# Kernel optimization log

Measured on AMD Instinct MI355X. Metric: run time of the kernel, lower is better.

The kernel has to match this reference:

```python
import jax, jax.numpy as jnp
import numpy as np

NODE_DIM = 512
HIDDEN = 4096
N_NODES = 4096  # must equal HIDDEN for pool Linear to typecheck (as in source)
N_EDGES = 131072


def setup_inputs() -> dict:
    key = jax.random.key(0)
    ks = jax.random.split(key, 12)
    s1 = 0.02
    x = jax.random.normal(ks[0], (N_NODES, NODE_DIM), dtype=jnp.float32)
    edge_index = jax.random.randint(ks[1], (2, N_EDGES), 0, N_NODES, dtype=jnp.int64)
    # encoder: Linear(node_dim, hidden) -> ReLU -> Linear(hidden, hidden)
    W1 = jax.random.normal(ks[2], (NODE_DIM, HIDDEN), dtype=jnp.float32) * s1
    b1 = jnp.zeros((HIDDEN,), dtype=jnp.float32)
    W2 = jax.random.normal(ks[3], (HIDDEN, HIDDEN), dtype=jnp.float32) * s1
    b2 = jnp.zeros((HIDDEN,), dtype=jnp.float32)
    # pool: Linear(hidden, hidden) -> ReLU -> Linear(hidden, 1)
    W3 = jax.random.normal(ks[4], (HIDDEN, HIDDEN), dtype=jnp.float32) * s1
    b3 = jnp.zeros((HIDDEN,), dtype=jnp.float32)
    W4 = jax.random.normal(ks[5], (HIDDEN, 1), dtype=jnp.float32) * s1
    b4 = jnp.zeros((1,), dtype=jnp.float32)
    return {"x": x, "edge_index": edge_index, "W1": W1, "b1": b1,
            "W2": W2, "b2": b2, "W3": W3, "b3": b3, "W4": W4, "b4": b4}


def reference(x, edge_index, W1, b1, W2, b2, W3, b3, W4, b4):
    # encoder MLP: [N, node_dim] -> [N, hidden]
    h = jax.nn.relu(x @ W1 + b1) @ W2 + b2
    # kernel_vector = (h @ h.T).sum(1) == h @ h.sum(0)  (avoids O(N^2) Gram)
    s = h.sum(axis=0)                 # [hidden]
    kernel_vector = h @ s             # [N]
    kv = kernel_vector[None, :]       # [1, N] with N == hidden
    pooled = jax.nn.relu(kv @ W3 + b3) @ W4 + b4   # [1, 1]
    return pooled
```

## Files before the change

kernel.cpp:

```cpp
#include <hip/hip_runtime.h>

#define NODES 4096
#define NDIM  512
#define HID   4096

typedef __attribute__((ext_vector_type(8))) short bf16x8;
typedef __attribute__((ext_vector_type(4))) float f32x4;

__device__ __forceinline__ float b2f(short v) {
  union { unsigned int u; float f; } c;
  c.u = ((unsigned int)(unsigned short)v) << 16;
  return c.f;
}
__device__ __forceinline__ short f2b(float f) {
  union { float f; unsigned int u; } c; c.f = f;
  unsigned int r = c.u + 0x7fffu + ((c.u >> 16) & 1u);
  return (short)(r >> 16);
}

__global__ __launch_bounds__(256) void k_prep(const float* __restrict__ x,
                                              const float* __restrict__ W1,
                                              const float* __restrict__ b2,
                                              const float* __restrict__ b3,
                                              short* __restrict__ xb,
                                              short* __restrict__ w1t,
                                              float* __restrict__ aacc,
                                              float* __restrict__ svec,
                                              float* __restrict__ uacc) {
  __shared__ float tile[32][33];
  int b = blockIdx.x;
  if (b < 2048) {
    int i = (b * 256 + threadIdx.x) * 4;
    float4 v = *(const float4*)(x + i);
    short4 o;
    o.x = f2b(v.x); o.y = f2b(v.y); o.z = f2b(v.z); o.w = f2b(v.w);
    *(short4*)(xb + i) = o;
  } else if (b < 4096) {
    int t = b - 2048;
    int n0 = (t & 127) * 32;
    int k0 = (t >> 7) * 32;
    int tx = threadIdx.x & 31, ty = threadIdx.x >> 5;
    #pragma unroll
    for (int j = 0; j < 4; ++j) {
      int kk = ty + j * 8;
      tile[kk][tx] = W1[(size_t)(k0 + kk) * HID + n0 + tx];
    }
    __syncthreads();
    #pragma unroll
    for (int j = 0; j < 4; ++j) {
      int nn = ty + j * 8;
      w1t[(size_t)(n0 + nn) * NDIM + k0 + tx] = f2b(tile[tx][nn]);
    }
  } else {
    int j = (b - 4096) * 256 + threadIdx.x;
    aacc[j] = 0.0f;
    svec[j] = (float)NODES * b2[j];
    uacc[j] = b3[j];
  }
}

__global__ __launch_bounds__(512, 2) void k_gemm1(const short* __restrict__ xb,
                                                  const short* __restrict__ w1t,
                                                  const float* __restrict__ b1,
                                                  short* __restrict__ Aout,
                                                  float* __restrict__ colsum) {
  extern __shared__ char smem[];
  __shared__ float csum[256];

  const int tid  = threadIdx.x;
  const int lane = tid & 63;
  const int wid  = tid >> 6;
  const int wr   = wid >> 2;
  const int wc   = wid & 3;

  int bswz = (blockIdx.x & 7) * 32 + (blockIdx.x >> 3);
  const int brow = (bswz >> 4) * 256, bcol = (bswz & 15) * 256;

  f32x4 acc[8][4];
  #pragma unroll
  for (int i = 0; i < 8; ++i)
    #pragma unroll
    for (int j = 0; j < 4; ++j)
      acc[i][j] = (f32x4){0.f, 0.f, 0.f, 0.f};

  if (tid < 256) csum[tid] = 0.f;

  const int fr = lane & 15;
  const int fko = ((lane >> 4) ^ ((lane >> 1) & 3)) * 8;

  const int off0 = tid * 16;
  const int row0 = off0 >> 6;
  const int gs   = (off0 >> 4) & 3;
  const int ce0  = (gs ^ ((row0 >> 1) & 3)) * 8;
  const short* gA0 = xb  + (size_t)(brow + row0) * NDIM + ce0;
  const short* gA1 = xb  + (size_t)(brow + row0 + 128) * NDIM + ce0;
  const short* gB0 = w1t + (size_t)(bcol + row0) * NDIM + ce0;
  const short* gB1 = w1t + (size_t)(bcol + row0 + 128) * NDIM + ce0;

#define GLOAD(src, dst) __builtin_amdgcn_global_load_lds( \
    (const __attribute__((address_space(1))) void*)(src), \
    (__attribute__((address_space(3))) void*)(dst), 16, 0, 0)

#define STAGE_HALF(buf, tile_, kh) do { \
    char* bA_ = smem + (buf) * 32768 + (kh) * 16384; \
    char* bB_ = smem + 65536 + (buf) * 32768 + (kh) * 16384; \
    int ks_ = (tile_) * 64 + (kh) * 32; \
    GLOAD(gA0 + ks_, bA_ + off0); \
    GLOAD(gA1 + ks_, bA_ + off0 + 8192); \
    GLOAD(gB0 + ks_, bB_ + off0); \
    GLOAD(gB1 + ks_, bB_ + off0 + 8192); \
  } while (0)

#define DS_BFR(buf, kh) do { \
    const short* Bb_ = (const short*)(smem + 65536 + (buf) * 32768 + (kh) * 16384); \
    _Pragma("unroll") \
    for (int ni = 0; ni < 4; ++ni) \
      bfr[ni] = *(const bf16x8*)(Bb_ + (wc * 64 + ni * 16 + fr) * 32 + fko); \
  } while (0)

#define DS_AF(buf, kh, mh) do { \
    const short* Ab_ = (const short*)(smem + (buf) * 32768 + (kh) * 16384); \
    _Pragma("unroll") \
    for (int mi = 0; mi < 4; ++mi) \
      af[mi] = *(const bf16x8*)(Ab_ + (wr * 128 + ((mh) * 4 + mi) * 16 + fr) * 32 + fko); \
  } while (0)

#define MFMA16(mh) do { \
    __builtin_amdgcn_s_setprio(1); \
    _Pragma("unroll") \
    for (int mi = 0; mi < 4; ++mi) \
      _Pragma("unroll") \
      for (int ni = 0; ni < 4; ++ni) \
        acc[(mh) * 4 + mi][ni] = __builtin_amdgcn_mfma_f32_16x16x32_bf16( \
            bfr[ni], af[mi], acc[(mh) * 4 + mi][ni], 0, 0, 0); \
    __builtin_amdgcn_s_setprio(0); \
  } while (0)

#define BAR() __builtin_amdgcn_s_barrier()
#define LGKM0() asm volatile("s_waitcnt lgkmcnt(0)" ::: "memory")
#define WCNT(s) asm volatile("s_waitcnt " s ::: "memory")

#define ITER(kk, DO_S0, DO_S2, V1, V3) do { \
    int b_ = (kk) & 1; \
    bf16x8 af[4], bfr[4]; \
     \
    if (DO_S0) STAGE_HALF(((kk) + 1) & 1, (kk) + 1, 1); \
    DS_BFR(b_, 0); DS_AF(b_, 0, 0); \
    BAR(); LGKM0(); \
    MFMA16(0); \
    BAR(); \
     \
    DS_AF(b_, 0, 1); \
    BAR(); LGKM0(); \
    MFMA16(1); \
    WCNT(V1); BAR(); \
     \
    if (DO_S2) STAGE_HALF(b_, (kk) + 2, 0); \
    DS_BFR(b_, 1); DS_AF(b_, 1, 0); \
    BAR(); LGKM0(); \
    MFMA16(0); \
    BAR(); \
     \
    DS_AF(b_, 1, 1); \
    BAR(); LGKM0(); \
    MFMA16(1); \
    WCNT(V3); BAR(); \
  } while (0)

  STAGE_HALF(0, 0, 0);
  STAGE_HALF(0, 0, 1);
  STAGE_HALF(1, 1, 0);
  WCNT("vmcnt(8)");
  BAR();

  #pragma unroll 1
  for (int kt = 0; kt < 6; ++kt)
    ITER(kt, true, true, "vmcnt(8)", "vmcnt(8)");
  ITER(6, true, false, "vmcnt(8)", "vmcnt(4)");
  ITER(7, false, false, "vmcnt(0)", "vmcnt(0)");

  const int cr = lane & 15;
  const int cg = (lane >> 4) * 4;
  float4 bias4[4];
  #pragma unroll
  for (int ni = 0; ni < 4; ++ni)
    bias4[ni] = *(const float4*)(b1 + bcol + wc * 64 + ni * 16 + cg);

  float cl[4][4];
  #pragma unroll
  for (int ni = 0; ni < 4; ++ni)
    #pragma unroll
    for (int r = 0; r < 4; ++r)
      cl[ni][r] = 0.f;

  short* pk = (short*)smem;
  #pragma unroll 1
  for (int half = 0; half < 2; ++half) {
    __syncthreads();
    if (wr == half) {
      #pragma unroll
      for (int mi = 0; mi < 8; ++mi) {
        int lrow = mi * 16 + cr;
        #pragma unroll
        for (int ni = 0; ni < 4; ++ni) {
          float v0 = fmaxf(acc[mi][ni][0] + bias4[ni].x, 0.f);
          float v1 = fmaxf(acc[mi][ni][1] + bias4[ni].y, 0.f);
          float v2 = fmaxf(acc[mi][ni][2] + bias4[ni].z, 0.f);
          float v3 = fmaxf(acc[mi][ni][3] + bias4[ni].w, 0.f);
          cl[ni][0] += v0; cl[ni][1] += v1; cl[ni][2] += v2; cl[ni][3] += v3;
          short4 o;
          o.x = f2b(v0); o.y = f2b(v1); o.z = f2b(v2); o.w = f2b(v3);
          *(short4*)(pk + lrow * 264 + wc * 64 + ni * 16 + cg) = o;
        }
      }
    }
    __syncthreads();
    #pragma unroll
    for (int i = 0; i < 8; ++i) {
      int c = tid + i * 512;
      int row = c >> 5, ch = c & 31;
      bf16x8 vv = *(const bf16x8*)(pk + row * 264 + ch * 8);
      *(bf16x8*)(Aout + (size_t)(brow + half * 128 + row) * HID + bcol + ch * 8) = vv;
    }
  }

  #pragma unroll
  for (int ni = 0; ni < 4; ++ni)
    #pragma unroll
    for (int r = 0; r < 4; ++r) {
      #pragma unroll
      for (int m = 1; m < 16; m <<= 1)
        cl[ni][r] += __shfl_xor(cl[ni][r], m);
    }
  if (cr == 0) {
    #pragma unroll
    for (int ni = 0; ni < 4; ++ni)
      #pragma unroll
      for (int r = 0; r < 4; ++r)
        atomicAdd(&csum[wc * 64 + ni * 16 + cg + r], cl[ni][r]);
  }
  __syncthreads();
  if (tid < 256) atomicAdd(&colsum[bcol + tid], csum[tid]);
}

__global__ __launch_bounds__(256) void k_gemv_at(const float* __restrict__ W,
                                                 const float* __restrict__ vin,
                                                 float* __restrict__ vout) {
  const int col = blockIdx.x * 1024 + threadIdx.x * 4;
  const int r0  = blockIdx.y * 64;
  float4 accv = {0.f, 0.f, 0.f, 0.f};
  const float* base = W + (size_t)r0 * HID + col;
  #pragma unroll 16
  for (int i = 0; i < 64; ++i) {
    float vi = vin[r0 + i];
    float4 wv = *(const float4*)(base + (size_t)i * HID);
    accv.x += vi * wv.x; accv.y += vi * wv.y;
    accv.z += vi * wv.z; accv.w += vi * wv.w;
  }
  atomicAdd(&vout[col + 0], accv.x);
  atomicAdd(&vout[col + 1], accv.y);
  atomicAdd(&vout[col + 2], accv.z);
  atomicAdd(&vout[col + 3], accv.w);
}

__global__ __launch_bounds__(256) void k_gemv_row(const float* __restrict__ W,
                                                  const float* __restrict__ vin,
                                                  const float* __restrict__ b2,
                                                  float* __restrict__ vout,
                                                  float* __restrict__ beta) {
  __shared__ float red[4];
  if (blockIdx.x == HID / 4) {
    float p = 0.f;
    for (int j = threadIdx.x; j < HID; j += 256) p += b2[j] * vin[j];
    #pragma unroll
    for (int o = 32; o > 0; o >>= 1) p += __shfl_down(p, o);
    int lane = threadIdx.x & 63, w = threadIdx.x >> 6;
    if (lane == 0) red[w] = p;
    __syncthreads();
    if (threadIdx.x == 0) beta[0] = red[0] + red[1] + red[2] + red[3];
    return;
  }
  int w = threadIdx.x >> 6, lane = threadIdx.x & 63;
  int row = blockIdx.x * 4 + w;
  const float* base = W + (size_t)row * HID;
  float p = 0.f;
  #pragma unroll 8
  for (int j = lane * 4; j < HID; j += 256) {
    float4 wv = *(const float4*)(base + j);
    float4 sv = *(const float4*)(vin + j);
    p += wv.x * sv.x + wv.y * sv.y + wv.z * sv.z + wv.w * sv.w;
  }
  #pragma unroll
  for (int o = 32; o > 0; o >>= 1) p += __shfl_down(p, o);
  if (lane == 0) vout[row] = p;
}

__global__ __launch_bounds__(256) void k_kv(const short* __restrict__ A,
                                            const float* __restrict__ t,
                                            const float* __restrict__ beta,
                                            float* __restrict__ kv) {
  int w = threadIdx.x >> 6, lane = threadIdx.x & 63;
  int row = blockIdx.x * 4 + w;
  const short* base = A + (size_t)row * HID;
  float p = 0.f;
  #pragma unroll
  for (int j = lane * 8; j < HID; j += 512) {
    bf16x8 av = *(const bf16x8*)(base + j);
    float4 t0 = *(const float4*)(t + j);
    float4 t1 = *(const float4*)(t + j + 4);
    p += b2f(av[0]) * t0.x + b2f(av[1]) * t0.y + b2f(av[2]) * t0.z + b2f(av[3]) * t0.w
       + b2f(av[4]) * t1.x + b2f(av[5]) * t1.y + b2f(av[6]) * t1.z + b2f(av[7]) * t1.w;
  }
  #pragma unroll
  for (int o = 32; o > 0; o >>= 1) p += __shfl_down(p, o);
  if (lane == 0) kv[row] = p + beta[0];
}

__global__ __launch_bounds__(256) void k_final(const float* __restrict__ uacc,
                                               const float* __restrict__ W4,
                                               const float* __restrict__ b4,
                                               float* __restrict__ out) {
  __shared__ float red[4];
  float p = 0.f;
  for (int j = threadIdx.x; j < HID; j += 256) {
    float uv = uacc[j];
    uv = uv > 0.f ? uv : 0.f;
    p += uv * W4[j];
  }
  #pragma unroll
  for (int o = 32; o > 0; o >>= 1) p += __shfl_down(p, o);
  int lane = threadIdx.x & 63, w = threadIdx.x >> 6;
  if (lane == 0) red[w] = p;
  __syncthreads();
  if (threadIdx.x == 0) out[0] = red[0] + red[1] + red[2] + red[3] + b4[0];
}

extern "C" void kernel_launch(void* const* d_in, const int* in_sizes, int n_in,
                              void* d_out, int out_size, void* d_ws, size_t ws_size,
                              hipStream_t stream) {
  const float* x  = (const float*)d_in[0];
  const float* W1 = (const float*)d_in[2];
  const float* b1 = (const float*)d_in[3];
  const float* W2 = (const float*)d_in[4];
  const float* b2 = (const float*)d_in[5];
  const float* W3 = (const float*)d_in[6];
  const float* b3 = (const float*)d_in[7];
  const float* W4 = (const float*)d_in[8];
  const float* b4 = (const float*)d_in[9];
  float* out = (float*)d_out;

  char* ws = (char*)d_ws;
  short* Abf  = (short*)(ws);
  short* xb   = (short*)(ws + 33554432);
  short* w1t  = (short*)(ws + 37748736);
  float* aacc = (float*)(ws + 41943040);
  float* svec = (float*)(ws + 41959424);
  float* tvec = (float*)(ws + 41975808);
  float* kvv  = (float*)(ws + 41992192);
  float* uacc = (float*)(ws + 42008576);
  float* beta = (float*)(ws + 42024960);

  k_prep    <<<dim3(4112),     dim3(256), 0, stream>>>(x, W1, b2, b3, xb, w1t, aacc, svec, uacc);
  k_gemm1   <<<dim3(256),      dim3(512), 131072, stream>>>(xb, w1t, b1, Abf, aacc);
  k_gemv_at <<<dim3(4, 64),    dim3(256), 0, stream>>>(W2, aacc, svec);
  k_gemv_row<<<dim3(1025),     dim3(256), 0, stream>>>(W2, svec, b2, tvec, beta);
  k_kv      <<<dim3(1024),     dim3(256), 0, stream>>>(Abf, tvec, beta, kvv);
  k_gemv_at <<<dim3(4, 64),    dim3(256), 0, stream>>>(W3, kvv, uacc);
  k_final   <<<dim3(1),        dim3(256), 0, stream>>>(uacc, W4, b4, out);
}
```

Measured before the change: 92.86 us.

## Fuse all stages into one cooperative persistent kernel with grid syncs

Merges the seven separate launches (prep, GEMM1, two gemv-transpose passes, row gemv, kv dot, final reduce) into one cooperative kernel of 256 blocks. Stages are separated by grid.sync() and the work in each stage is remapped onto the fixed grid. The aim is to remove launch gaps and kernel boundaries between the many small memory-bound stages. In exchange, every stage is limited to 256 blocks of 512 threads, and each grid-wide barrier has its own cost.

```diff
diff --git a/kernel.cpp b/kernel.cpp
--- a/kernel.cpp
+++ b/kernel.cpp
@@ -1,4 +1,7 @@
 #include <hip/hip_runtime.h>
+#include <hip/hip_cooperative_groups.h>
+
+namespace cg = cooperative_groups;
 
 #define NODES 4096
 #define NDIM  512
@@ -18,84 +21,82 @@
   return (short)(r >> 16);
 }
 
-__global__ __launch_bounds__(256) void k_prep(const float* __restrict__ x,
-                                              const float* __restrict__ W1,
-                                              const float* __restrict__ b2,
-                                              const float* __restrict__ b3,
-                                              short* __restrict__ xb,
-                                              short* __restrict__ w1t,
-                                              float* __restrict__ aacc,
-                                              float* __restrict__ svec,
-                                              float* __restrict__ uacc) {
-  __shared__ float tile[32][33];
-  int b = blockIdx.x;
-  if (b < 2048) {
-    int i = (b * 256 + threadIdx.x) * 4;
-    float4 v = *(const float4*)(x + i);
-    short4 o;
-    o.x = f2b(v.x); o.y = f2b(v.y); o.z = f2b(v.z); o.w = f2b(v.w);
-    *(short4*)(xb + i) = o;
-  } else if (b < 4096) {
-    int t = b - 2048;
-    int n0 = (t & 127) * 32;
-    int k0 = (t >> 7) * 32;
-    int tx = threadIdx.x & 31, ty = threadIdx.x >> 5;
-    #pragma unroll
-    for (int j = 0; j < 4; ++j) {
-      int kk = ty + j * 8;
-      tile[kk][tx] = W1[(size_t)(k0 + kk) * HID + n0 + tx];
-    }
-    __syncthreads();
-    #pragma unroll
-    for (int j = 0; j < 4; ++j) {
-      int nn = ty + j * 8;
-      w1t[(size_t)(n0 + nn) * NDIM + k0 + tx] = f2b(tile[tx][nn]);
-    }
-  } else {
-    int j = (b - 4096) * 256 + threadIdx.x;
-    aacc[j] = 0.0f;
-    svec[j] = (float)NODES * b2[j];
-    uacc[j] = b3[j];
-  }
-}
-
-__global__ __launch_bounds__(512, 2) void k_gemm1(const short* __restrict__ xb,
-                                                  const short* __restrict__ w1t,
-                                                  const float* __restrict__ b1,
-                                                  short* __restrict__ Aout,
-                                                  float* __restrict__ colsum) {
+__global__ __launch_bounds__(512, 2) void k_mega(
+    const float* __restrict__ x,  const float* __restrict__ W1,
+    const float* __restrict__ W2, const float* __restrict__ W3,
+    const float* __restrict__ b1, const float* __restrict__ b2,
+    const float* __restrict__ b3, const float* __restrict__ W4,
+    const float* __restrict__ b4,
+    short* __restrict__ xb, short* __restrict__ w1t, short* __restrict__ Abf,
+    float* __restrict__ aacc, float* __restrict__ svec, float* __restrict__ tvec,
+    float* __restrict__ kvv, float* __restrict__ uacc, float* __restrict__ beta,
+    float* __restrict__ out) {
   extern __shared__ char smem[];
   __shared__ float csum[256];
+  __shared__ float red[8];
+  cg::grid_group grid = cg::this_grid();
 
   const int tid  = threadIdx.x;
   const int lane = tid & 63;
   const int wid  = tid >> 6;
-  const int wr   = wid >> 2;
-  const int wc   = wid & 3;
-
-  int bswz = (blockIdx.x & 7) * 32 + (blockIdx.x >> 3);
-  const int brow = (bswz >> 4) * 256, bcol = (bswz & 15) * 256;
-
-  f32x4 acc[8][4];
-  #pragma unroll
-  for (int i = 0; i < 8; ++i)
-    #pragma unroll
-    for (int j = 0; j < 4; ++j)
-      acc[i][j] = (f32x4){0.f, 0.f, 0.f, 0.f};
-
-  if (tid < 256) csum[tid] = 0.f;
-
-  const int fr = lane & 15;
-  const int fko = ((lane >> 4) ^ ((lane >> 1) & 3)) * 8;
-
-  const int off0 = tid * 16;
-  const int row0 = off0 >> 6;
-  const int gs   = (off0 >> 4) & 3;
-  const int ce0  = (gs ^ ((row0 >> 1) & 3)) * 8;
-  const short* gA0 = xb  + (size_t)(brow + row0) * NDIM + ce0;
-  const short* gA1 = xb  + (size_t)(brow + row0 + 128) * NDIM + ce0;
-  const short* gB0 = w1t + (size_t)(bcol + row0) * NDIM + ce0;
-  const short* gB1 = w1t + (size_t)(bcol + row0 + 128) * NDIM + ce0;
+  const int gtid = blockIdx.x * 512 + tid;
+
+  {
+    for (int i = gtid; i < NODES * NDIM / 4; i += 131072) {
+      float4 v = *(const float4*)(x + (size_t)i * 4);
+      short4 o;
+      o.x = f2b(v.x); o.y = f2b(v.y); o.z = f2b(v.z); o.w = f2b(v.w);
+      *(short4*)(xb + (size_t)i * 4) = o;
+    }
+    float* tl = (float*)smem + wid * (32 * 34);
+    int t = blockIdx.x * 8 + wid;
+    int n0 = (t & 127) * 32, k0 = (t >> 7) * 32;
+    int tx = lane & 31, ty = lane >> 5;
+    #pragma unroll
+    for (int j = 0; j < 16; ++j) {
+      int kk = ty + j * 2;
+      tl[kk * 34 + tx] = W1[(size_t)(k0 + kk) * HID + n0 + tx];
+    }
+    __syncthreads();
+    #pragma unroll
+    for (int j = 0; j < 16; ++j) {
+      int nn = ty + j * 2;
+      w1t[(size_t)(n0 + nn) * NDIM + k0 + tx] = f2b(tl[tx * 34 + nn]);
+    }
+    if (gtid < HID) {
+      aacc[gtid] = 0.f;
+      svec[gtid] = (float)NODES * b2[gtid];
+      uacc[gtid] = b3[gtid];
+    }
+  }
+  grid.sync();
+
+  {
+    const int wr = wid >> 2;
+    const int wc = wid & 3;
+    int bswz = (blockIdx.x & 7) * 32 + (blockIdx.x >> 3);
+    const int brow = (bswz >> 4) * 256, bcol = (bswz & 15) * 256;
+
+    f32x4 acc[8][4];
+    #pragma unroll
+    for (int i = 0; i < 8; ++i)
+      #pragma unroll
+      for (int j = 0; j < 4; ++j)
+        acc[i][j] = (f32x4){0.f, 0.f, 0.f, 0.f};
+
+    if (tid < 256) csum[tid] = 0.f;
+
+    const int fr  = lane & 15;
+    const int fko = ((lane >> 4) ^ ((lane >> 1) & 3)) * 8;
+
+    const int off0 = tid * 16;
+    const int row0 = off0 >> 6;
+    const int gs   = (off0 >> 4) & 3;
+    const int ce0  = (gs ^ ((row0 >> 1) & 3)) * 8;
+    const short* gA0 = xb  + (size_t)(brow + row0) * NDIM + ce0;
+    const short* gA1 = xb  + (size_t)(brow + row0 + 128) * NDIM + ce0;
+    const short* gB0 = w1t + (size_t)(bcol + row0) * NDIM + ce0;
+    const short* gB1 = w1t + (size_t)(bcol + row0 + 128) * NDIM + ce0;
 
 #define GLOAD(src, dst) __builtin_amdgcn_global_load_lds( \
     (const __attribute__((address_space(1))) void*)(src), \
@@ -143,196 +144,224 @@
 #define ITER(kk, DO_S0, DO_S2, V1, V3) do { \
     int b_ = (kk) & 1; \
     bf16x8 af[4], bfr[4]; \
-     \
     if (DO_S0) STAGE_HALF(((kk) + 1) & 1, (kk) + 1, 1); \
     DS_BFR(b_, 0); DS_AF(b_, 0, 0); \
     BAR(); LGKM0(); \
     MFMA16(0); \
     BAR(); \
-     \
     DS_AF(b_, 0, 1); \
     BAR(); LGKM0(); \
     MFMA16(1); \
     WCNT(V1); BAR(); \
-     \
     if (DO_S2) STAGE_HALF(b_, (kk) + 2, 0); \
     DS_BFR(b_, 1); DS_AF(b_, 1, 0); \
     BAR(); LGKM0(); \
     MFMA16(0); \
     BAR(); \
-     \
     DS_AF(b_, 1, 1); \
     BAR(); LGKM0(); \
     MFMA16(1); \
     WCNT(V3); BAR(); \
   } while (0)
 
-  STAGE_HALF(0, 0, 0);
-  STAGE_HALF(0, 0, 1);
-  STAGE_HALF(1, 1, 0);
-  WCNT("vmcnt(8)");
-  BAR();
-
-  #pragma unroll 1
-  for (int kt = 0; kt < 6; ++kt)
-    ITER(kt, true, true, "vmcnt(8)", "vmcnt(8)");
-  ITER(6, true, false, "vmcnt(8)", "vmcnt(4)");
-  ITER(7, false, false, "vmcnt(0)", "vmcnt(0)");
-
-  const int cr = lane & 15;
-  const int cg = (lane >> 4) * 4;
-  float4 bias4[4];
-  #pragma unroll
-  for (int ni = 0; ni < 4; ++ni)
-    bias4[ni] = *(const float4*)(b1 + bcol + wc * 64 + ni * 16 + cg);
-
-  float cl[4][4];
-  #pragma unroll
-  for (int ni = 0; ni < 4; ++ni)
-    #pragma unroll
-    for (int r = 0; r < 4; ++r)
-      cl[ni][r] = 0.f;
-
-  short* pk = (short*)smem;
-  #pragma unroll 1
-  for (int half = 0; half < 2; ++half) {
-    __syncthreads();
-    if (wr == half) {
-      #pragma unroll
-      for (int mi = 0; mi < 8; ++mi) {
-        int lrow = mi * 16 + cr;
+    STAGE_HALF(0, 0, 0);
+    STAGE_HALF(0, 0, 1);
+    STAGE_HALF(1, 1, 0);
+    WCNT("vmcnt(8)");
+    BAR();
+
+    #pragma unroll 1
+    for (int kt = 0; kt < 6; ++kt)
+      ITER(kt, true, true, "vmcnt(8)", "vmcnt(8)");
+    ITER(6, true, false, "vmcnt(8)", "vmcnt(4)");
+    ITER(7, false, false, "vmcnt(0)", "vmcnt(0)");
+
+    const int cr = lane & 15;
+    const int cg = (lane >> 4) * 4;
+    float4 bias4[4];
+    #pragma unroll
+    for (int ni = 0; ni < 4; ++ni)
+      bias4[ni] = *(const float4*)(b1 + bcol + wc * 64 + ni * 16 + cg);
+
+    float cl[4][4];
+    #pragma unroll
+    for (int ni = 0; ni < 4; ++ni)
+      #pragma unroll
+      for (int r = 0; r < 4; ++r)
+        cl[ni][r] = 0.f;
+
+    short* pk = (short*)smem;
+    #pragma unroll 1
+    for (int half = 0; half < 2; ++half) {
+      __syncthreads();
+      if (wr == half) {
         #pragma unroll
-        for (int ni = 0; ni < 4; ++ni) {
-          float v0 = fmaxf(acc[mi][ni][0] + bias4[ni].x, 0.f);
-          float v1 = fmaxf(acc[mi][ni][1] + bias4[ni].y, 0.f);
-          float v2 = fmaxf(acc[mi][ni][2] + bias4[ni].z, 0.f);
-          float v3 = fmaxf(acc[mi][ni][3] + bias4[ni].w, 0.f);
-          cl[ni][0] += v0; cl[ni][1] += v1; cl[ni][2] += v2; cl[ni][3] += v3;
-          short4 o;
-          o.x = f2b(v0); o.y = f2b(v1); o.z = f2b(v2); o.w = f2b(v3);
-          *(short4*)(pk + lrow * 264 + wc * 64 + ni * 16 + cg) = o;
+        for (int mi = 0; mi < 8; ++mi) {
+          int lrow = mi * 16 + cr;
+          #pragma unroll
+          for (int ni = 0; ni < 4; ++ni) {
+            float v0 = fmaxf(acc[mi][ni][0] + bias4[ni].x, 0.f);
+            float v1 = fmaxf(acc[mi][ni][1] + bias4[ni].y, 0.f);
+            float v2 = fmaxf(acc[mi][ni][2] + bias4[ni].z, 0.f);
+            float v3 = fmaxf(acc[mi][ni][3] + bias4[ni].w, 0.f);
+            cl[ni][0] += v0; cl[ni][1] += v1; cl[ni][2] += v2; cl[ni][3] += v3;
+            short4 o;
+            o.x = f2b(v0); o.y = f2b(v1); o.z = f2b(v2); o.w = f2b(v3);
+            *(short4*)(pk + lrow * 264 + wc * 64 + ni * 16 + cg) = o;
+          }
         }
       }
+      __syncthreads();
+      #pragma unroll
+      for (int i = 0; i < 8; ++i) {
+        int c = tid + i * 512;
+        int row = c >> 5, ch = c & 31;
+        bf16x8 vv = *(const bf16x8*)(pk + row * 264 + ch * 8);
+        *(bf16x8*)(Abf + (size_t)(brow + half * 128 + row) * HID + bcol + ch * 8) = vv;
+      }
+    }
+
+    #pragma unroll
+    for (int ni = 0; ni < 4; ++ni)
+      #pragma unroll
+      for (int r = 0; r < 4; ++r) {
+        #pragma unroll
+        for (int m = 1; m < 16; m <<= 1)
+          cl[ni][r] += __shfl_xor(cl[ni][r], m);
+      }
+    if (cr == 0) {
+      #pragma unroll
+      for (int ni = 0; ni < 4; ++ni)
+        #pragma unroll
+        for (int r = 0; r < 4; ++r)
+          atomicAdd(&csum[wc * 64 + ni * 16 + cg + r], cl[ni][r]);
     }
     __syncthreads();
-    #pragma unroll
-    for (int i = 0; i < 8; ++i) {
-      int c = tid + i * 512;
-      int row = c >> 5, ch = c & 31;
-      bf16x8 vv = *(const bf16x8*)(pk + row * 264 + ch * 8);
-      *(bf16x8*)(Aout + (size_t)(brow + half * 128 + row) * HID + bcol + ch * 8) = vv;
-    }
-  }
-
-  #pragma unroll
-  for (int ni = 0; ni < 4; ++ni)
-    #pragma unroll
-    for (int r = 0; r < 4; ++r) {
-      #pragma unroll
-      for (int m = 1; m < 16; m <<= 1)
-        cl[ni][r] += __shfl_xor(cl[ni][r], m);
-    }
-  if (cr == 0) {
-    #pragma unroll
-    for (int ni = 0; ni < 4; ++ni)
-      #pragma unroll
-      for (int r = 0; r < 4; ++r)
-        atomicAdd(&csum[wc * 64 + ni * 16 + cg + r], cl[ni][r]);
-  }
-  __syncthreads();
-  if (tid < 256) atomicAdd(&colsum[bcol + tid], csum[tid]);
-}
-
-__global__ __launch_bounds__(256) void k_gemv_at(const float* __restrict__ W,
-                                                 const float* __restrict__ vin,
-                                                 float* __restrict__ vout) {
-  const int col = blockIdx.x * 1024 + threadIdx.x * 4;
-  const int r0  = blockIdx.y * 64;
-  float4 accv = {0.f, 0.f, 0.f, 0.f};
-  const float* base = W + (size_t)r0 * HID + col;
-  #pragma unroll 16
-  for (int i = 0; i < 64; ++i) {
-    float vi = vin[r0 + i];
-    float4 wv = *(const float4*)(base + (size_t)i * HID);
-    accv.x += vi * wv.x; accv.y += vi * wv.y;
-    accv.z += vi * wv.z; accv.w += vi * wv.w;
-  }
-  atomicAdd(&vout[col + 0], accv.x);
-  atomicAdd(&vout[col + 1], accv.y);
-  atomicAdd(&vout[col + 2], accv.z);
-  atomicAdd(&vout[col + 3], accv.w);
-}
-
-__global__ __launch_bounds__(256) void k_gemv_row(const float* __restrict__ W,
-                                                  const float* __restrict__ vin,
-                                                  const float* __restrict__ b2,
-                                                  float* __restrict__ vout,
-                                                  float* __restrict__ beta) {
-  __shared__ float red[4];
-  if (blockIdx.x == HID / 4) {
+    if (tid < 256) atomicAdd(&aacc[bcol + tid], csum[tid]);
+  }
+  grid.sync();
+
+  {
+    int vb = blockIdx.x * 2 + (tid >> 8);
+    int vt = tid & 255;
+    int col = (vb & 3) * 1024 + vt * 4;
+    int r0  = (vb >> 2) * 32;
+    float4 a4 = {0.f, 0.f, 0.f, 0.f};
+    const float* base = W2 + (size_t)r0 * HID + col;
+    #pragma unroll 16
+    for (int i = 0; i < 32; ++i) {
+      float vi = aacc[r0 + i];
+      float4 wv = *(const float4*)(base + (size_t)i * HID);
+      a4.x += vi * wv.x; a4.y += vi * wv.y;
+      a4.z += vi * wv.z; a4.w += vi * wv.w;
+    }
+    atomicAdd(&svec[col + 0], a4.x);
+    atomicAdd(&svec[col + 1], a4.y);
+    atomicAdd(&svec[col + 2], a4.z);
+    atomicAdd(&svec[col + 3], a4.w);
+  }
+  grid.sync();
+
+  {
+    int wg = blockIdx.x * 8 + wid;
+    const float* base0 = W2 + (size_t)(wg * 2) * HID;
+    const float* base1 = base0 + HID;
+    float p0 = 0.f, p1 = 0.f;
+    #pragma unroll 4
+    for (int j = lane * 4; j < HID; j += 256) {
+      float4 s4 = *(const float4*)(svec + j);
+      float4 w0 = *(const float4*)(base0 + j);
+      float4 w1v = *(const float4*)(base1 + j);
+      p0 += w0.x * s4.x + w0.y * s4.y + w0.z * s4.z + w0.w * s4.w;
+      p1 += w1v.x * s4.x + w1v.y * s4.y + w1v.z * s4.z + w1v.w * s4.w;
+    }
+    #pragma unroll
+    for (int o = 32; o > 0; o >>= 1) {
+      p0 += __shfl_down(p0, o);
+      p1 += __shfl_down(p1, o);
+    }
+    if (lane == 0) {
+      tvec[wg * 2]     = p0;
+      tvec[wg * 2 + 1] = p1;
+    }
+    if (wg == 0) {
+      float p = 0.f;
+      for (int j = lane; j < HID; j += 64) p += b2[j] * svec[j];
+      #pragma unroll
+      for (int o = 32; o > 0; o >>= 1) p += __shfl_down(p, o);
+      if (lane == 0) beta[0] = p;
+    }
+  }
+  grid.sync();
+
+  {
+    int wg = blockIdx.x * 8 + wid;
+    const short* base0 = Abf + (size_t)(wg * 2) * HID;
+    const short* base1 = base0 + HID;
+    float p0 = 0.f, p1 = 0.f;
+    #pragma unroll
+    for (int j = lane * 8; j < HID; j += 512) {
+      bf16x8 a0 = *(const bf16x8*)(base0 + j);
+      bf16x8 a1 = *(const bf16x8*)(base1 + j);
+      float4 t0 = *(const float4*)(tvec + j);
+      float4 t1 = *(const float4*)(tvec + j + 4);
+      p0 += b2f(a0[0]) * t0.x + b2f(a0[1]) * t0.y + b2f(a0[2]) * t0.z + b2f(a0[3]) * t0.w
+          + b2f(a0[4]) * t1.x + b2f(a0[5]) * t1.y + b2f(a0[6]) * t1.z + b2f(a0[7]) * t1.w;
+      p1 += b2f(a1[0]) * t0.x + b2f(a1[1]) * t0.y + b2f(a1[2]) * t0.z + b2f(a1[3]) * t0.w
+          + b2f(a1[4]) * t1.x + b2f(a1[5]) * t1.y + b2f(a1[6]) * t1.z + b2f(a1[7]) * t1.w;
+    }
+    #pragma unroll
+    for (int o = 32; o > 0; o >>= 1) {
+      p0 += __shfl_down(p0, o);
+      p1 += __shfl_down(p1, o);
+    }
+    if (lane == 0) {
+      float bb = beta[0];
+      kvv[wg * 2]     = p0 + bb;
+      kvv[wg * 2 + 1] = p1 + bb;
+    }
+  }
+  grid.sync();
+
+  {
+    int vb = blockIdx.x * 2 + (tid >> 8);
+    int vt = tid & 255;
+    int col = (vb & 3) * 1024 + vt * 4;
+    int r0  = (vb >> 2) * 32;
+    float4 a4 = {0.f, 0.f, 0.f, 0.f};
+    const float* base = W3 + (size_t)r0 * HID + col;
+    #pragma unroll 16
+    for (int i = 0; i < 32; ++i) {
+      float vi = kvv[r0 + i];
+      float4 wv = *(const float4*)(base + (size_t)i * HID);
+      a4.x += vi * wv.x; a4.y += vi * wv.y;
+      a4.z += vi * wv.z; a4.w += vi * wv.w;
+    }
+    atomicAdd(&uacc[col + 0], a4.x);
+    atomicAdd(&uacc[col + 1], a4.y);
+    atomicAdd(&uacc[col + 2], a4.z);
+    atomicAdd(&uacc[col + 3], a4.w);
+  }
+  grid.sync();
+
+  if (blockIdx.x == 0) {
     float p = 0.f;
-    for (int j = threadIdx.x; j < HID; j += 256) p += b2[j] * vin[j];
+    for (int j = tid; j < HID; j += 512) {
+      float u = uacc[j];
+      u = u > 0.f ? u : 0.f;
+      p += u * W4[j];
+    }
     #pragma unroll
     for (int o = 32; o > 0; o >>= 1) p += __shfl_down(p, o);
-    int lane = threadIdx.x & 63, w = threadIdx.x >> 6;
-    if (lane == 0) red[w] = p;
+    if (lane == 0) red[wid] = p;
     __syncthreads();
-    if (threadIdx.x == 0) beta[0] = red[0] + red[1] + red[2] + red[3];
-    return;
-  }
-  int w = threadIdx.x >> 6, lane = threadIdx.x & 63;
-  int row = blockIdx.x * 4 + w;
-  const float* base = W + (size_t)row * HID;
-  float p = 0.f;
-  #pragma unroll 8
-  for (int j = lane * 4; j < HID; j += 256) {
-    float4 wv = *(const float4*)(base + j);
-    float4 sv = *(const float4*)(vin + j);
-    p += wv.x * sv.x + wv.y * sv.y + wv.z * sv.z + wv.w * sv.w;
-  }
-  #pragma unroll
-  for (int o = 32; o > 0; o >>= 1) p += __shfl_down(p, o);
-  if (lane == 0) vout[row] = p;
-}
-
-__global__ __launch_bounds__(256) void k_kv(const short* __restrict__ A,
-                                            const float* __restrict__ t,
-                                            const float* __restrict__ beta,
-                                            float* __restrict__ kv) {
-  int w = threadIdx.x >> 6, lane = threadIdx.x & 63;
-  int row = blockIdx.x * 4 + w;
-  const short* base = A + (size_t)row * HID;
-  float p = 0.f;
-  #pragma unroll
-  for (int j = lane * 8; j < HID; j += 512) {
-    bf16x8 av = *(const bf16x8*)(base + j);
-    float4 t0 = *(const float4*)(t + j);
-    float4 t1 = *(const float4*)(t + j + 4);
-    p += b2f(av[0]) * t0.x + b2f(av[1]) * t0.y + b2f(av[2]) * t0.z + b2f(av[3]) * t0.w
-       + b2f(av[4]) * t1.x + b2f(av[5]) * t1.y + b2f(av[6]) * t1.z + b2f(av[7]) * t1.w;
-  }
-  #pragma unroll
-  for (int o = 32; o > 0; o >>= 1) p += __shfl_down(p, o);
-  if (lane == 0) kv[row] = p + beta[0];
-}
-
-__global__ __launch_bounds__(256) void k_final(const float* __restrict__ uacc,
-                                               const float* __restrict__ W4,
-                                               const float* __restrict__ b4,
-                                               float* __restrict__ out) {
-  __shared__ float red[4];
-  float p = 0.f;
-  for (int j = threadIdx.x; j < HID; j += 256) {
-    float uv = uacc[j];
-    uv = uv > 0.f ? uv : 0.f;
-    p += uv * W4[j];
-  }
-  #pragma unroll
-  for (int o = 32; o > 0; o >>= 1) p += __shfl_down(p, o);
-  int lane = threadIdx.x & 63, w = threadIdx.x >> 6;
-  if (lane == 0) red[w] = p;
-  __syncthreads();
-  if (threadIdx.x == 0) out[0] = red[0] + red[1] + red[2] + red[3] + b4[0];
+    if (tid == 0) {
+      float s = 0.f;
+      #pragma unroll
+      for (int i = 0; i < 8; ++i) s += red[i];
+      out[0] = s + b4[0];
+    }
+  }
 }
 
 extern "C" void kernel_launch(void* const* d_in, const int* in_sizes, int n_in,
@@ -360,11 +389,12 @@
   float* uacc = (float*)(ws + 42008576);
   float* beta = (float*)(ws + 42024960);
 
-  k_prep    <<<dim3(4112),     dim3(256), 0, stream>>>(x, W1, b2, b3, xb, w1t, aacc, svec, uacc);
-  k_gemm1   <<<dim3(256),      dim3(512), 131072, stream>>>(xb, w1t, b1, Abf, aacc);
-  k_gemv_at <<<dim3(4, 64),    dim3(256), 0, stream>>>(W2, aacc, svec);
-  k_gemv_row<<<dim3(1025),     dim3(256), 0, stream>>>(W2, svec, b2, tvec, beta);
-  k_kv      <<<dim3(1024),     dim3(256), 0, stream>>>(Abf, tvec, beta, kvv);
-  k_gemv_at <<<dim3(4, 64),    dim3(256), 0, stream>>>(W3, kvv, uacc);
-  k_final   <<<dim3(1),        dim3(256), 0, stream>>>(uacc, W4, b4, out);
+  void* args[] = {
+    (void*)&x, (void*)&W1, (void*)&W2, (void*)&W3, (void*)&b1, (void*)&b2,
+    (void*)&b3, (void*)&W4, (void*)&b4, (void*)&xb, (void*)&w1t, (void*)&Abf,
+    (void*)&aacc, (void*)&svec, (void*)&tvec, (void*)&kvv, (void*)&uacc,
+    (void*)&beta, (void*)&out
+  };
+  hipLaunchCooperativeKernel((const void*)k_mega, dim3(256), dim3(512),
+                             args, 131072, stream);
 }
```

Measured after the change: 288.1 us. +210.3%, slower.
